# Kernel tuning notes

Hardware: AMD Instinct MI355X
Metric: run time of the kernel (lower is better)

## Reference

```python
import jax, jax.numpy as jnp
import numpy as np

BN_EPS = 1e-5
NN_EPS = 1e-8


def _conv_bn_relu(x, w, gamma, beta, mean, var):
    # x: (B, Cin, N), w: (Cout, Cin) -- 1x1 Conv1d (no bias) + BatchNorm1d (eval) + ReLU
    y = jnp.einsum('oc,bcn->bon', w, x)
    scale = gamma / jnp.sqrt(var + BN_EPS)            # (Cout,)
    shift = beta - mean * scale                       # (Cout,)
    return jax.nn.relu(y * scale[:, None] + shift[:, None])


def setup_inputs() -> dict:
    key = jax.random.key(0)
    ks = jax.random.split(key, 10)
    B, N, M = 4, 2048, 8192
    Cin, Cout = 512, 256
    inp = {
        'x1': jax.random.normal(ks[0], (B, Cin, N), dtype=jnp.float32),
        'p1': jax.random.uniform(ks[1], (B, N, 3), dtype=jnp.float32) * 4.0,
        'x2': jax.random.normal(ks[2], (B, Cout, M), dtype=jnp.float32),
        'p2': jax.random.uniform(ks[3], (B, M, 3), dtype=jnp.float32) * 4.0,
        # up_mlp params
        'w_up': jax.random.normal(ks[4], (Cout, Cin), dtype=jnp.float32) * (1.0 / np.sqrt(Cin)),
        'g_up': jnp.ones((Cout,), jnp.float32),
        'b_up': jnp.zeros((Cout,), jnp.float32),
        'm_up': jax.random.normal(ks[5], (Cout,), dtype=jnp.float32) * 0.1,
        'v_up': jax.random.uniform(ks[6], (Cout,), dtype=jnp.float32) + 0.5,
        # lateral_mlp params
        'w_lat': jax.random.normal(ks[7], (Cout, Cout), dtype=jnp.float32) * (1.0 / np.sqrt(Cout)),
        'g_lat': jnp.ones((Cout,), jnp.float32),
        'b_lat': jnp.zeros((Cout,), jnp.float32),
        'm_lat': jax.random.normal(ks[8], (Cout,), dtype=jnp.float32) * 0.1,
        'v_lat': jax.random.uniform(ks[9], (Cout,), dtype=jnp.float32) + 0.5,
    }
    return inp


def reference(x1, p1, x2, p2, w_up, g_up, b_up, m_up, v_up,
              w_lat, g_lat, b_lat, m_lat, v_lat):
    # up branch: conv1x1 + BN + ReLU on coarse features  (B, Cout, N)
    f1 = _conv_bn_relu(x1, w_up, g_up, b_up, m_up, v_up)

    # three_nn: for each fine point p2 find 3 nearest coarse points p1 (squared dist)
    d2 = (jnp.sum(p2 * p2, -1)[:, :, None]
          + jnp.sum(p1 * p1, -1)[:, None, :]
          - 2.0 * jnp.einsum('bmd,bnd->bmn', p2, p1))        # (B, M, N)
    d2 = jnp.maximum(d2, 0.0)
    neg_d, idx = jax.lax.top_k(-d2, 3)                       # (B, M, 3)
    dist = -neg_d

    # inverse-distance weights
    dist_recip = 1.0 / (dist + NN_EPS)
    weight = dist_recip / jnp.sum(dist_recip, axis=2, keepdims=True)  # (B, M, 3)

    # three_interpolate: gather + weighted sum
    gathered = jax.vmap(lambda f, i: f[:, i])(f1, idx)       # (B, Cout, M, 3)
    interp = jnp.einsum('bcmk,bmk->bcm', gathered, weight)   # (B, Cout, M)

    # lateral branch
    f2 = _conv_bn_relu(x2, w_lat, g_lat, b_lat, m_lat, v_lat)

    return interp + f2, p2
```

## Files before the change

### kernel.cpp

```cpp
#include <hip/hip_runtime.h>
#include <math.h>
#include <float.h>

#define B_    4
#define N_    2048
#define M_    8192
#define CIN_  512
#define COUT_ 256

typedef __attribute__((ext_vector_type(8))) short short8v;
typedef __attribute__((ext_vector_type(4))) float f32x4;

__device__ __forceinline__ void ws_store_f32(float* p, float v) {
    __hip_atomic_store((unsigned int*)p, __float_as_uint(v),
                       __ATOMIC_RELAXED, __HIP_MEMORY_SCOPE_SYSTEM);
}
__device__ __forceinline__ void ws_store_u32(int* p, int v) {
    __hip_atomic_store((unsigned int*)p, (unsigned int)v,
                       __ATOMIC_RELAXED, __HIP_MEMORY_SCOPE_SYSTEM);
}

__global__ __launch_bounds__(64) void inv_kernel() {
    asm volatile("buffer_inv sc0 sc1" ::: "memory");
}

__device__ __forceinline__ unsigned short f2bf(float f) {
    unsigned u = __float_as_uint(f);
    u += 0x7fffu + ((u >> 16) & 1u);
    return (unsigned short)(u >> 16);
}

template<int K, int MODE>
__device__ __forceinline__ void gemm_body(
    char* raw, int b, int c0, int m0,
    const float* __restrict__ X, const float* __restrict__ W,
    const float* __restrict__ gam, const float* __restrict__ bet,
    const float* __restrict__ mu, const float* __restrict__ var,
    float* __restrict__ dst,
    const float* __restrict__ f1t, const float* __restrict__ nnrec, int Mdim)
{
    char* Ab = raw;
    char* Bb = raw + 10240;

    const int tid = threadIdx.x;
    const int l  = tid & 63;
    const int wv = tid >> 6;
    const int wc = wv & 1, wn = wv >> 1;

    f32x4 acc[4][4];
    #pragma unroll
    for (int i = 0; i < 4; ++i)
        #pragma unroll
        for (int j = 0; j < 4; ++j)
            acc[i][j] = (f32x4){0.f, 0.f, 0.f, 0.f};

    const int ksA = tid & 7;
    const int crA = tid >> 3;
    const int kqB = tid >> 5;
    const int mlB = tid & 31;

    float4 wreg[4];
    float  xreg[4][4];
    #pragma unroll
    for (int r = 0; r < 4; ++r)
        wreg[r] = *(const float4*)(W + (size_t)(c0 + crA + 32 * r) * K + ksA * 4);
    #pragma unroll
    for (int jj = 0; jj < 4; ++jj) {
        const float* xp = X + ((size_t)b * K + kqB * 4) * Mdim + m0 + mlB + 32 * jj;
        xreg[jj][0] = xp[0];
        xreg[jj][1] = xp[(size_t)Mdim];
        xreg[jj][2] = xp[(size_t)2 * Mdim];
        xreg[jj][3] = xp[(size_t)3 * Mdim];
    }

    for (int kc = 0; kc < K; kc += 32) {
        #pragma unroll
        for (int r = 0; r < 4; ++r) {
            unsigned lo = f2bf(wreg[r].x) | ((unsigned)f2bf(wreg[r].y) << 16);
            unsigned hi = f2bf(wreg[r].z) | ((unsigned)f2bf(wreg[r].w) << 16);
            *(uint2*)(Ab + (crA + 32 * r) * 80 + ksA * 8) = make_uint2(lo, hi);
        }
        #pragma unroll
        for (int jj = 0; jj < 4; ++jj) {
            unsigned lo = f2bf(xreg[jj][0]) | ((unsigned)f2bf(xreg[jj][1]) << 16);
            unsigned hi = f2bf(xreg[jj][2]) | ((unsigned)f2bf(xreg[jj][3]) << 16);
            *(uint2*)(Bb + (mlB + 32 * jj) * 80 + kqB * 8) = make_uint2(lo, hi);
        }
        if (kc + 32 < K) {
            #pragma unroll
            for (int r = 0; r < 4; ++r)
                wreg[r] = *(const float4*)(W + (size_t)(c0 + crA + 32 * r) * K + (kc + 32) + ksA * 4);
            #pragma unroll
            for (int jj = 0; jj < 4; ++jj) {
                const float* xp = X + ((size_t)b * K + (kc + 32) + kqB * 4) * Mdim + m0 + mlB + 32 * jj;
                xreg[jj][0] = xp[0];
                xreg[jj][1] = xp[(size_t)Mdim];
                xreg[jj][2] = xp[(size_t)2 * Mdim];
                xreg[jj][3] = xp[(size_t)3 * Mdim];
            }
        }
        __syncthreads();
        short8v a[4], bfv[4];
        #pragma unroll
        for (int ci = 0; ci < 4; ++ci)
            a[ci] = *(const short8v*)(Ab + (wc * 64 + ci * 16 + (l & 15)) * 80 + (l >> 4) * 16);
        #pragma unroll
        for (int ni = 0; ni < 4; ++ni)
            bfv[ni] = *(const short8v*)(Bb + (wn * 64 + ni * 16 + (l & 15)) * 80 + (l >> 4) * 16);
        #pragma unroll
        for (int ci = 0; ci < 4; ++ci)
            #pragma unroll
            for (int ni = 0; ni < 4; ++ni)
                acc[ci][ni] = __builtin_amdgcn_mfma_f32_16x16x32_bf16(
                    a[ci], bfv[ni], acc[ci][ni], 0, 0, 0);
        __syncthreads();
    }

    const int lc = (l >> 4) * 4;
    float scA[4][4], shA[4][4];
    #pragma unroll
    for (int ci = 0; ci < 4; ++ci)
        #pragma unroll
        for (int r = 0; r < 4; ++r) {
            int c = c0 + wc * 64 + ci * 16 + lc + r;
            float sc = gam[c] / sqrtf(var[c] + 1e-5f);
            scA[ci][r] = sc;
            shA[ci][r] = bet[c] - mu[c] * sc;
        }

    if constexpr (MODE == 0) {
        float* S = (float*)raw;
        #pragma unroll
        for (int h = 0; h < 2; ++h) {
            if (wn == h) {
                #pragma unroll
                for (int ni = 0; ni < 4; ++ni)
                    #pragma unroll
                    for (int ci = 0; ci < 4; ++ci)
                        #pragma unroll
                        for (int r = 0; r < 4; ++r)
                            S[(ni * 16 + (l & 15)) * 133 + wc * 64 + ci * 16 + lc + r] =
                                fmaxf(acc[ci][ni][r] * scA[ci][r] + shA[ci][r], 0.f);
            }
            __syncthreads();
            #pragma unroll
            for (int i = 0; i < 32; ++i) {
                int e = tid + i * 256;
                int row = e >> 7, c = e & 127;
                ws_store_f32(dst + ((size_t)b * N_ + m0 + h * 64 + row) * COUT_ + c0 + c,
                             S[row * 133 + c]);
            }
            __syncthreads();
        }
    } else {
        #pragma unroll
        for (int ni = 0; ni < 4; ++ni) {
            int mg = m0 + wn * 64 + ni * 16 + (l & 15);
            const float* rp = nnrec + ((size_t)b * M_ + mg) * 8;
            float4 ra = *(const float4*)rp;
            float2 rb = *(const float2*)(rp + 4);
            int   i0 = __float_as_int(ra.x);
            int   i1 = __float_as_int(ra.y);
            int   i2 = __float_as_int(ra.z);
            float w0 = ra.w, w1 = rb.x, w2 = rb.y;
            const float4* g0 = (const float4*)(f1t + ((size_t)b * N_ + i0) * COUT_ + c0 + wc * 64 + lc);
            const float4* g1 = (const float4*)(f1t + ((size_t)b * N_ + i1) * COUT_ + c0 + wc * 64 + lc);
            const float4* g2 = (const float4*)(f1t + ((size_t)b * N_ + i2) * COUT_ + c0 + wc * 64 + lc);
            #pragma unroll
            for (int ci = 0; ci < 4; ++ci) {
                float4 G0 = g0[ci * 4];
                float4 G1 = g1[ci * 4];
                float4 G2 = g2[ci * 4];
                const float* f0 = (const float*)&G0;
                const float* f1 = (const float*)&G1;
                const float* f2 = (const float*)&G2;
                #pragma unroll
                for (int r = 0; r < 4; ++r) {
                    float v = fmaxf(acc[ci][ni][r] * scA[ci][r] + shA[ci][r], 0.f);
                    v = fmaf(w0, f0[r], v);
                    v = fmaf(w1, f1[r], v);
                    v = fmaf(w2, f2[r], v);
                    int c = c0 + wc * 64 + ci * 16 + lc + r;
                    dst[((size_t)b * COUT_ + c) * M_ + mg] = v;
                }
            }
        }
    }
}

__global__ __launch_bounds__(256) void up_kernel(
    const float* __restrict__ x1, const float* __restrict__ w_up,
    const float* __restrict__ g_up, const float* __restrict__ b_up,
    const float* __restrict__ m_up, const float* __restrict__ v_up,
    float* __restrict__ f1t)
{
    __shared__ float4 raw4[2130];
    gemm_body<CIN_, 0>((char*)raw4, blockIdx.z, blockIdx.y * 128, blockIdx.x * 128,
                       x1, w_up, g_up, b_up, m_up, v_up, f1t,
                       nullptr, nullptr, N_);
}

__global__ __launch_bounds__(256) void lat_kernel(
    const float* __restrict__ x2, const float* __restrict__ w_lat,
    const float* __restrict__ g_lat, const float* __restrict__ b_lat,
    const float* __restrict__ m_lat, const float* __restrict__ v_lat,
    const float* __restrict__ f1t, const float* __restrict__ nnrec,
    float* __restrict__ out0)
{
    __shared__ float4 raw4[1280];
    gemm_body<COUT_, 1>((char*)raw4, blockIdx.z, blockIdx.y * 128, blockIdx.x * 128,
                        x2, w_lat, g_lat, b_lat, m_lat, v_lat, out0,
                        f1t, nnrec, M_);
}

__device__ __forceinline__ void lex_insert(float e, int j,
    float& D0, float& D1, float& D2, int& I0, int& I1, int& I2)
{
    bool l0 = (e < D0) || (e == D0 && j < I0);
    bool l1 = (e < D1) || (e == D1 && j < I1);
    bool l2 = (e < D2) || (e == D2 && j < I2);
    if (l2) {
        if (l0)      { D2=D1; I2=I1; D1=D0; I1=I0; D0=e; I0=j; }
        else if (l1) { D2=D1; I2=I1; D1=e;  I1=j; }
        else         { D2=e;  I2=j; }
    }
}

__device__ __forceinline__ void bubble_insert(float e, int ie,
    float& D0, float& D1, float& D2, int& I0, int& I1, int& I2)
{
    bool l2 = e < D2;
    D2 = l2 ? e  : D2;
    I2 = l2 ? ie : I2;
    bool s1 = D2 < D1;
    float tf = D1; int ti = I1;
    D1 = s1 ? D2 : D1;  I1 = s1 ? I2 : I1;
    D2 = s1 ? tf : D2;  I2 = s1 ? ti : I2;
    bool s0 = D1 < D0;
    tf = D0; ti = I0;
    D0 = s0 ? D1 : D0;  I0 = s0 ? I1 : I0;
    D1 = s0 ? tf : D1;  I1 = s0 ? ti : I1;
}

__global__ __launch_bounds__(256) void three_nn_kernel(
    const float* __restrict__ p1, const float* __restrict__ p2,
    float* __restrict__ nnrec, float* __restrict__ out1)
{
    __shared__ float4 P[8][257];
    const int b = blockIdx.y;
    #pragma unroll
    for (int r = 0; r < 8; ++r) {
        int n = r * 256 + threadIdx.x;
        float x = p1[((size_t)(b*N_)+n)*3 + 0];
        float y = p1[((size_t)(b*N_)+n)*3 + 1];
        float z = p1[((size_t)(b*N_)+n)*3 + 2];
        float t = x * x;
        t = fmaf(y, y, t);
        t = fmaf(z, z, t);
        P[r][threadIdx.x] = make_float4(x, y, z, t);
    }
    __syncthreads();

    const int m = blockIdx.x * 32 + (threadIdx.x >> 3);
    const int s = threadIdx.x & 7;
    const size_t pbase = ((size_t)(b*M_) + m) * 3;
    const float qx = p2[pbase+0], qy = p2[pbase+1], qz = p2[pbase+2];
    float s2 = qx * qx;
    s2 = fmaf(qy, qy, s2);
    s2 = fmaf(qz, qz, s2);

    float D0 = FLT_MAX, D1 = FLT_MAX, D2 = FLT_MAX;
    int   I0 = 0x7fffffff, I1 = 0x7fffffff, I2 = 0x7fffffff;
    const int base = s * 256;
    const float4* Ps = &P[s][0];

    float4 ca[8], cb[8];
    #pragma unroll
    for (int u = 0; u < 8; ++u) ca[u] = Ps[u];

    #define PROC(CV, IB)                                                     \
        {                                                                    \
            float d[8];                                                      \
            _Pragma("unroll")                                                \
            for (int u = 0; u < 8; ++u) {                                    \
                float dot = qx * CV[u].x;                                    \
                dot = fmaf(qy, CV[u].y, dot);                                \
                dot = fmaf(qz, CV[u].z, dot);                                \
                float d2 = fmaf(-2.0f, dot, s2 + CV[u].w);                   \
                d[u] = fmaxf(d2, 0.0f);                                      \
            }                                                                \
            _Pragma("unroll")                                                \
            for (int u = 0; u < 8; ++u)                                      \
                bubble_insert(d[u], (IB) + u, D0, D1, D2, I0, I1, I2);       \
        }

    for (int j = 0; j < 32; j += 2) {
        #pragma unroll
        for (int u = 0; u < 8; ++u) cb[u] = Ps[(j + 1) * 8 + u];
        PROC(ca, base + j * 8);
        if (j + 2 < 32) {
            #pragma unroll
            for (int u = 0; u < 8; ++u) ca[u] = Ps[(j + 2) * 8 + u];
        }
        PROC(cb, base + (j + 1) * 8);
    }
    #undef PROC

    #pragma unroll
    for (int st = 1; st <= 4; st <<= 1) {
        float E0 = __shfl_xor(D0, st), E1 = __shfl_xor(D1, st), E2 = __shfl_xor(D2, st);
        int   J0 = __shfl_xor(I0, st), J1 = __shfl_xor(I1, st), J2 = __shfl_xor(I2, st);
        lex_insert(E0, J0, D0, D1, D2, I0, I1, I2);
        lex_insert(E1, J1, D0, D1, D2, I0, I1, I2);
        lex_insert(E2, J2, D0, D1, D2, I0, I1, I2);
    }
    if (s == 0) {
        float r0 = 1.0f / (D0 + 1e-8f);
        float r1 = 1.0f / (D1 + 1e-8f);
        float r2 = 1.0f / (D2 + 1e-8f);
        float sum = (r0 + r1) + r2;
        float* rp = nnrec + ((size_t)(b*M_) + m) * 8;
        ws_store_u32((int*)rp + 0, I0);
        ws_store_u32((int*)rp + 1, I1);
        ws_store_u32((int*)rp + 2, I2);
        ws_store_f32(rp + 3, r0 / sum);
        ws_store_f32(rp + 4, r1 / sum);
        ws_store_f32(rp + 5, r2 / sum);
        size_t o = ((size_t)(b*M_) + m) * 3;
        out1[o+0] = qx; out1[o+1] = qy; out1[o+2] = qz;
    }
}

extern "C" void kernel_launch(void* const* d_in, const int* in_sizes, int n_in,
                              void* d_out, int out_size, void* d_ws, size_t ws_size,
                              hipStream_t stream)
{
    (void)in_sizes; (void)n_in; (void)out_size; (void)ws_size;

    const float* x1    = (const float*)d_in[0];
    const float* p1    = (const float*)d_in[1];
    const float* x2    = (const float*)d_in[2];
    const float* p2    = (const float*)d_in[3];
    const float* w_up  = (const float*)d_in[4];
    const float* g_up  = (const float*)d_in[5];
    const float* b_up  = (const float*)d_in[6];
    const float* m_up  = (const float*)d_in[7];
    const float* v_up  = (const float*)d_in[8];
    const float* w_lat = (const float*)d_in[9];
    const float* g_lat = (const float*)d_in[10];
    const float* b_lat = (const float*)d_in[11];
    const float* m_lat = (const float*)d_in[12];
    const float* v_lat = (const float*)d_in[13];

    float* out0 = (float*)d_out;
    float* out1 = out0 + (size_t)B_ * COUT_ * M_;

    float* f1t   = (float*)d_ws;
    float* nnrec = (float*)((char*)d_ws + (size_t)B_ * N_ * COUT_ * 4);

    up_kernel<<<dim3(N_ / 128, COUT_ / 128, B_), 256, 0, stream>>>(
        x1, w_up, g_up, b_up, m_up, v_up, f1t);

    three_nn_kernel<<<dim3(M_ / 32, B_), 256, 0, stream>>>(
        p1, p2, nnrec, out1);

    inv_kernel<<<dim3(512), 64, 0, stream>>>();

    lat_kernel<<<dim3(M_ / 128, COUT_ / 128, B_), 256, 0, stream>>>(
        x2, w_lat, g_lat, b_lat, m_lat, v_lat, f1t, nnrec, out0);
}
```

Before: 103.4 us.

## Halve GEMM channel tile, prefetch NN records, split top-3 into independent chains

The GEMM kernels shrink their output-channel tile from 128 to 64. This doubles the grid size and cuts accumulator registers and LDS use, aiming for more occupancy and parallelism, at the cost of reloading the X tile for twice as many blocks. The lateral kernel now loads the nearest-neighbour index/weight records before the GEMM loop so their latency overlaps the MMA work. The three_nn kernel keeps four independent top-3 lists instead of one serial bubble-insert chain, then merges them, to expose more instruction-level parallelism at the cost of extra registers.

```diff
diff --git a/kernel.cpp b/kernel.cpp
--- a/kernel.cpp
+++ b/kernel.cpp
@@ -40,16 +40,16 @@
     const float* __restrict__ f1t, const float* __restrict__ nnrec, int Mdim)
 {
     char* Ab = raw;
-    char* Bb = raw + 10240;
+    char* Bb = raw + 5120;
 
     const int tid = threadIdx.x;
     const int l  = tid & 63;
     const int wv = tid >> 6;
     const int wc = wv & 1, wn = wv >> 1;
 
-    f32x4 acc[4][4];
-    #pragma unroll
-    for (int i = 0; i < 4; ++i)
+    f32x4 acc[2][4];
+    #pragma unroll
+    for (int i = 0; i < 2; ++i)
         #pragma unroll
         for (int j = 0; j < 4; ++j)
             acc[i][j] = (f32x4){0.f, 0.f, 0.f, 0.f};
@@ -59,10 +59,21 @@
     const int kqB = tid >> 5;
     const int mlB = tid & 31;
 
-    float4 wreg[4];
+    float4 ra[4]; float2 rb[4];
+    if constexpr (MODE == 1) {
+        #pragma unroll
+        for (int ni = 0; ni < 4; ++ni) {
+            int mg = m0 + wn * 64 + ni * 16 + (l & 15);
+            const float* rp = nnrec + ((size_t)b * M_ + mg) * 8;
+            ra[ni] = *(const float4*)rp;
+            rb[ni] = *(const float2*)(rp + 4);
+        }
+    }
+
+    float4 wreg[2];
     float  xreg[4][4];
     #pragma unroll
-    for (int r = 0; r < 4; ++r)
+    for (int r = 0; r < 2; ++r)
         wreg[r] = *(const float4*)(W + (size_t)(c0 + crA + 32 * r) * K + ksA * 4);
     #pragma unroll
     for (int jj = 0; jj < 4; ++jj) {
@@ -75,7 +86,7 @@
 
     for (int kc = 0; kc < K; kc += 32) {
         #pragma unroll
-        for (int r = 0; r < 4; ++r) {
+        for (int r = 0; r < 2; ++r) {
             unsigned lo = f2bf(wreg[r].x) | ((unsigned)f2bf(wreg[r].y) << 16);
             unsigned hi = f2bf(wreg[r].z) | ((unsigned)f2bf(wreg[r].w) << 16);
             *(uint2*)(Ab + (crA + 32 * r) * 80 + ksA * 8) = make_uint2(lo, hi);
@@ -88,7 +99,7 @@
         }
         if (kc + 32 < K) {
             #pragma unroll
-            for (int r = 0; r < 4; ++r)
+            for (int r = 0; r < 2; ++r)
                 wreg[r] = *(const float4*)(W + (size_t)(c0 + crA + 32 * r) * K + (kc + 32) + ksA * 4);
             #pragma unroll
             for (int jj = 0; jj < 4; ++jj) {
@@ -100,15 +111,15 @@
             }
         }
         __syncthreads();
-        short8v a[4], bfv[4];
-        #pragma unroll
-        for (int ci = 0; ci < 4; ++ci)
-            a[ci] = *(const short8v*)(Ab + (wc * 64 + ci * 16 + (l & 15)) * 80 + (l >> 4) * 16);
+        short8v a[2], bfv[4];
+        #pragma unroll
+        for (int ci = 0; ci < 2; ++ci)
+            a[ci] = *(const short8v*)(Ab + (wc * 32 + ci * 16 + (l & 15)) * 80 + (l >> 4) * 16);
         #pragma unroll
         for (int ni = 0; ni < 4; ++ni)
             bfv[ni] = *(const short8v*)(Bb + (wn * 64 + ni * 16 + (l & 15)) * 80 + (l >> 4) * 16);
         #pragma unroll
-        for (int ci = 0; ci < 4; ++ci)
+        for (int ci = 0; ci < 2; ++ci)
             #pragma unroll
             for (int ni = 0; ni < 4; ++ni)
                 acc[ci][ni] = __builtin_amdgcn_mfma_f32_16x16x32_bf16(
@@ -117,12 +128,12 @@
     }
 
     const int lc = (l >> 4) * 4;
-    float scA[4][4], shA[4][4];
-    #pragma unroll
-    for (int ci = 0; ci < 4; ++ci)
+    float scA[2][4], shA[2][4];
+    #pragma unroll
+    for (int ci = 0; ci < 2; ++ci)
         #pragma unroll
         for (int r = 0; r < 4; ++r) {
-            int c = c0 + wc * 64 + ci * 16 + lc + r;
+            int c = c0 + wc * 32 + ci * 16 + lc + r;
             float sc = gam[c] / sqrtf(var[c] + 1e-5f);
             scA[ci][r] = sc;
             shA[ci][r] = bet[c] - mu[c] * sc;
@@ -136,19 +147,19 @@
                 #pragma unroll
                 for (int ni = 0; ni < 4; ++ni)
                     #pragma unroll
-                    for (int ci = 0; ci < 4; ++ci)
+                    for (int ci = 0; ci < 2; ++ci)
                         #pragma unroll
                         for (int r = 0; r < 4; ++r)
-                            S[(ni * 16 + (l & 15)) * 133 + wc * 64 + ci * 16 + lc + r] =
+                            S[(ni * 16 + (l & 15)) * 66 + wc * 32 + ci * 16 + lc + r] =
                                 fmaxf(acc[ci][ni][r] * scA[ci][r] + shA[ci][r], 0.f);
             }
             __syncthreads();
             #pragma unroll
-            for (int i = 0; i < 32; ++i) {
+            for (int i = 0; i < 16; ++i) {
                 int e = tid + i * 256;
-                int row = e >> 7, c = e & 127;
+                int row = e >> 6, c = e & 63;
                 ws_store_f32(dst + ((size_t)b * N_ + m0 + h * 64 + row) * COUT_ + c0 + c,
-                             S[row * 133 + c]);
+                             S[row * 66 + c]);
             }
             __syncthreads();
         }
@@ -156,18 +167,15 @@
         #pragma unroll
         for (int ni = 0; ni < 4; ++ni) {
             int mg = m0 + wn * 64 + ni * 16 + (l & 15);
-            const float* rp = nnrec + ((size_t)b * M_ + mg) * 8;
-            float4 ra = *(const float4*)rp;
-            float2 rb = *(const float2*)(rp + 4);
-            int   i0 = __float_as_int(ra.x);
-            int   i1 = __float_as_int(ra.y);
-            int   i2 = __float_as_int(ra.z);
-            float w0 = ra.w, w1 = rb.x, w2 = rb.y;
-            const float4* g0 = (const float4*)(f1t + ((size_t)b * N_ + i0) * COUT_ + c0 + wc * 64 + lc);
-            const float4* g1 = (const float4*)(f1t + ((size_t)b * N_ + i1) * COUT_ + c0 + wc * 64 + lc);
-            const float4* g2 = (const float4*)(f1t + ((size_t)b * N_ + i2) * COUT_ + c0 + wc * 64 + lc);
-            #pragma unroll
-            for (int ci = 0; ci < 4; ++ci) {
+            int   i0 = __float_as_int(ra[ni].x);
+            int   i1 = __float_as_int(ra[ni].y);
+            int   i2 = __float_as_int(ra[ni].z);
+            float w0 = ra[ni].w, w1 = rb[ni].x, w2 = rb[ni].y;
+            const float4* g0 = (const float4*)(f1t + ((size_t)b * N_ + i0) * COUT_ + c0 + wc * 32 + lc);
+            const float4* g1 = (const float4*)(f1t + ((size_t)b * N_ + i1) * COUT_ + c0 + wc * 32 + lc);
+            const float4* g2 = (const float4*)(f1t + ((size_t)b * N_ + i2) * COUT_ + c0 + wc * 32 + lc);
+            #pragma unroll
+            for (int ci = 0; ci < 2; ++ci) {
                 float4 G0 = g0[ci * 4];
                 float4 G1 = g1[ci * 4];
                 float4 G2 = g2[ci * 4];
@@ -180,7 +188,7 @@
                     v = fmaf(w0, f0[r], v);
                     v = fmaf(w1, f1[r], v);
                     v = fmaf(w2, f2[r], v);
-                    int c = c0 + wc * 64 + ci * 16 + lc + r;
+                    int c = c0 + wc * 32 + ci * 16 + lc + r;
                     dst[((size_t)b * COUT_ + c) * M_ + mg] = v;
                 }
             }
@@ -194,8 +202,8 @@
     const float* __restrict__ m_up, const float* __restrict__ v_up,
     float* __restrict__ f1t)
 {
-    __shared__ float4 raw4[2130];
-    gemm_body<CIN_, 0>((char*)raw4, blockIdx.z, blockIdx.y * 128, blockIdx.x * 128,
+    __shared__ float4 raw4[1056];
+    gemm_body<CIN_, 0>((char*)raw4, blockIdx.z, blockIdx.y * 64, blockIdx.x * 128,
                        x1, w_up, g_up, b_up, m_up, v_up, f1t,
                        nullptr, nullptr, N_);
 }
@@ -207,8 +215,8 @@
     const float* __restrict__ f1t, const float* __restrict__ nnrec,
     float* __restrict__ out0)
 {
-    __shared__ float4 raw4[1280];
-    gemm_body<COUT_, 1>((char*)raw4, blockIdx.z, blockIdx.y * 128, blockIdx.x * 128,
+    __shared__ float4 raw4[960];
+    gemm_body<COUT_, 1>((char*)raw4, blockIdx.z, blockIdx.y * 64, blockIdx.x * 128,
                         x2, w_lat, g_lat, b_lat, m_lat, v_lat, out0,
                         f1t, nnrec, M_);
 }
@@ -269,42 +277,48 @@
     s2 = fmaf(qy, qy, s2);
     s2 = fmaf(qz, qz, s2);
 
-    float D0 = FLT_MAX, D1 = FLT_MAX, D2 = FLT_MAX;
-    int   I0 = 0x7fffffff, I1 = 0x7fffffff, I2 = 0x7fffffff;
+    float D0a, D1a, D2a, D0b, D1b, D2b, D0c, D1c, D2c, D0d, D1d, D2d;
+    int   I0a, I1a, I2a, I0b, I1b, I2b, I0c, I1c, I2c, I0d, I1d, I2d;
+    D0a=D1a=D2a=D0b=D1b=D2b=D0c=D1c=D2c=D0d=D1d=D2d=FLT_MAX;
+    I0a=I1a=I2a=I0b=I1b=I2b=I0c=I1c=I2c=I0d=I1d=I2d=0x7fffffff;
+
     const int base = s * 256;
     const float4* Ps = &P[s][0];
 
-    float4 ca[8], cb[8];
-    #pragma unroll
-    for (int u = 0; u < 8; ++u) ca[u] = Ps[u];
-
-    #define PROC(CV, IB)                                                     \
-        {                                                                    \
-            float d[8];                                                      \
-            _Pragma("unroll")                                                \
-            for (int u = 0; u < 8; ++u) {                                    \
-                float dot = qx * CV[u].x;                                    \
-                dot = fmaf(qy, CV[u].y, dot);                                \
-                dot = fmaf(qz, CV[u].z, dot);                                \
-                float d2 = fmaf(-2.0f, dot, s2 + CV[u].w);                   \
-                d[u] = fmaxf(d2, 0.0f);                                      \
-            }                                                                \
-            _Pragma("unroll")                                                \
-            for (int u = 0; u < 8; ++u)                                      \
-                bubble_insert(d[u], (IB) + u, D0, D1, D2, I0, I1, I2);       \
-        }
-
-    for (int j = 0; j < 32; j += 2) {
-        #pragma unroll
-        for (int u = 0; u < 8; ++u) cb[u] = Ps[(j + 1) * 8 + u];
-        PROC(ca, base + j * 8);
-        if (j + 2 < 32) {
-            #pragma unroll
-            for (int u = 0; u < 8; ++u) ca[u] = Ps[(j + 2) * 8 + u];
-        }
-        PROC(cb, base + (j + 1) * 8);
-    }
-    #undef PROC
+    for (int t = 0; t < 256; t += 8) {
+        float4 c[8];
+        #pragma unroll
+        for (int u = 0; u < 8; ++u) c[u] = Ps[t + u];
+        float d[8];
+        #pragma unroll
+        for (int u = 0; u < 8; ++u) {
+            float dot = qx * c[u].x;
+            dot = fmaf(qy, c[u].y, dot);
+            dot = fmaf(qz, c[u].z, dot);
+            float d2 = fmaf(-2.0f, dot, s2 + c[u].w);
+            d[u] = fmaxf(d2, 0.0f);
+        }
+        bubble_insert(d[0], base + t + 0, D0a, D1a, D2a, I0a, I1a, I2a);
+        bubble_insert(d[1], base + t + 1, D0b, D1b, D2b, I0b, I1b, I2b);
+        bubble_insert(d[2], base + t + 2, D0c, D1c, D2c, I0c, I1c, I2c);
+        bubble_insert(d[3], base + t + 3, D0d, D1d, D2d, I0d, I1d, I2d);
+        bubble_insert(d[4], base + t + 4, D0a, D1a, D2a, I0a, I1a, I2a);
+        bubble_insert(d[5], base + t + 5, D0b, D1b, D2b, I0b, I1b, I2b);
+        bubble_insert(d[6], base + t + 6, D0c, D1c, D2c, I0c, I1c, I2c);
+        bubble_insert(d[7], base + t + 7, D0d, D1d, D2d, I0d, I1d, I2d);
+    }
+
+    float D0 = D0a, D1 = D1a, D2 = D2a;
+    int   I0 = I0a, I1 = I1a, I2 = I2a;
+    lex_insert(D0b, I0b, D0, D1, D2, I0, I1, I2);
+    lex_insert(D1b, I1b, D0, D1, D2, I0, I1, I2);
+    lex_insert(D2b, I2b, D0, D1, D2, I0, I1, I2);
+    lex_insert(D0c, I0c, D0, D1, D2, I0, I1, I2);
+    lex_insert(D1c, I1c, D0, D1, D2, I0, I1, I2);
+    lex_insert(D2c, I2c, D0, D1, D2, I0, I1, I2);
+    lex_insert(D0d, I0d, D0, D1, D2, I0, I1, I2);
+    lex_insert(D1d, I1d, D0, D1, D2, I0, I1, I2);
+    lex_insert(D2d, I2d, D0, D1, D2, I0, I1, I2);
 
     #pragma unroll
     for (int st = 1; st <= 4; st <<= 1) {
@@ -358,7 +372,7 @@
     float* f1t   = (float*)d_ws;
     float* nnrec = (float*)((char*)d_ws + (size_t)B_ * N_ * COUT_ * 4);
 
-    up_kernel<<<dim3(N_ / 128, COUT_ / 128, B_), 256, 0, stream>>>(
+    up_kernel<<<dim3(N_ / 128, COUT_ / 64, B_), 256, 0, stream>>>(
         x1, w_up, g_up, b_up, m_up, v_up, f1t);
 
     three_nn_kernel<<<dim3(M_ / 32, B_), 256, 0, stream>>>(
@@ -366,6 +380,6 @@
 
     inv_kernel<<<dim3(512), 64, 0, stream>>>();
 
-    lat_kernel<<<dim3(M_ / 128, COUT_ / 128, B_), 256, 0, stream>>>(
+    lat_kernel<<<dim3(M_ / 128, COUT_ / 64, B_), 256, 0, stream>>>(
         x2, w_lat, g_lat, b_lat, m_lat, v_lat, f1t, nnrec, out0);
 }
```

After: 100.4 us. -2.9%, faster.
